# Kernel optimization log

Hardware: AMD Instinct MI355X
Metric: run time of the kernel (lower is better)

Reference implementation:

```python
import jax, jax.numpy as jnp
import numpy as np

N_NODES = 50000
N_EDGES = 400000
F_IN = 128
HID = 64
HEADS = 8
N_CLASSES = 16
NEG_SLOPE = 0.2  # PyG GATConv default negative_slope


def _glorot(key, shape):
    fan_in, fan_out = shape[0], shape[-1]
    lim = jnp.sqrt(6.0 / (fan_in + fan_out))
    return jax.random.uniform(key, shape, jnp.float32, -lim, lim)


def setup_inputs() -> dict:
    key = jax.random.key(0)
    ks = jax.random.split(key, 16)
    x = jax.random.normal(ks[0], (N_NODES, F_IN), jnp.float32)
    edge_index = jax.random.randint(ks[1], (2, N_EDGES), 0, N_NODES, jnp.int64)
    # layer 0: F_IN -> HEADS*HID (concat)
    W0 = _glorot(ks[2], (F_IN, HEADS * HID))
    a_s0 = _glorot(ks[3], (HEADS, HID))
    a_d0 = _glorot(ks[4], (HEADS, HID))
    b0 = jnp.zeros((HEADS * HID,), jnp.float32)
    # layer 1: HEADS*HID -> HEADS*HID (concat)
    W1 = _glorot(ks[5], (HEADS * HID, HEADS * HID))
    a_s1 = _glorot(ks[6], (HEADS, HID))
    a_d1 = _glorot(ks[7], (HEADS, HID))
    b1 = jnp.zeros((HEADS * HID,), jnp.float32)
    # final layer: HEADS*HID -> N_CLASSES, heads=1, concat=False (mean over heads)
    W2 = _glorot(ks[8], (HEADS * HID, 1 * N_CLASSES))
    a_s2 = _glorot(ks[9], (1, N_CLASSES))
    a_d2 = _glorot(ks[10], (1, N_CLASSES))
    b2 = jnp.zeros((N_CLASSES,), jnp.float32)
    return {"x": x, "edge_index": edge_index,
            "W0": W0, "a_s0": a_s0, "a_d0": a_d0, "b0": b0,
            "W1": W1, "a_s1": a_s1, "a_d1": a_d1, "b1": b1,
            "W2": W2, "a_s2": a_s2, "a_d2": a_d2, "b2": b2}


def gat_conv(x, src, dst, W, a_src, a_dst, b, num_nodes, concat):
    """One PyG-style GATConv (self-loops already in src/dst).
    x: [N, F_in]; W: [F_in, H*C]; a_src/a_dst: [H, C]; b: [H*C] or [C]."""
    H, C = a_src.shape
    h = (x @ W).reshape(num_nodes, H, C)                    # [N,H,C]
    al_s = jnp.einsum('nhc,hc->nh', h, a_src)               # [N,H]
    al_d = jnp.einsum('nhc,hc->nh', h, a_dst)               # [N,H]
    e = jax.nn.leaky_relu(al_s[src] + al_d[dst], NEG_SLOPE) # [E,H]
    # scatter-softmax over incoming edges of each destination node
    m = jax.ops.segment_max(e, dst, num_segments=num_nodes)  # [N,H]
    ex = jnp.exp(e - m[dst])
    denom = jax.ops.segment_sum(ex, dst, num_segments=num_nodes)
    alpha = ex / denom[dst]                                  # [E,H]
    out = jax.ops.segment_sum(alpha[:, :, None] * h[src], dst,
                              num_segments=num_nodes)        # [N,H,C]
    if concat:
        return out.reshape(num_nodes, H * C) + b
    return out.mean(axis=1) + b


def reference(x, edge_index, W0, a_s0, a_d0, b0, W1, a_s1, a_d1, b1,
              W2, a_s2, a_d2, b2):
    N = x.shape[0]
    # PyG GATConv adds self-loops by default
    loops = jnp.arange(N, dtype=edge_index.dtype)
    src = jnp.concatenate([edge_index[0], loops])
    dst = jnp.concatenate([edge_index[1], loops])
    h = gat_conv(x, src, dst, W0, a_s0, a_d0, b0, N, concat=True)
    h = jax.nn.elu(h)  # dropout is identity in eval mode
    h = gat_conv(h, src, dst, W1, a_s1, a_d1, b1, N, concat=True)
    h = jax.nn.elu(h)
    return gat_conv(h, src, dst, W2, a_s2, a_d2, b2, N, concat=False)
```

## Files before the change

kernel.cpp:

```cpp
#include <hip/hip_runtime.h>

#define N_NODES 50000
#define N_EDGES 400000
#define E_TOT   450000
#define NEG 0.2f
#define NB_SCAN ((N_NODES + 255) / 256)
#define MAXD 64

typedef unsigned short ushort_t;
typedef __attribute__((ext_vector_type(8))) _Float16 half8;
typedef __attribute__((ext_vector_type(4))) float  f32x4;
typedef __attribute__((ext_vector_type(8))) unsigned short ushort8;

__device__ __forceinline__ ushort_t f2h(float f){
    _Float16 h = (_Float16)f;
    union { _Float16 h; ushort_t u; } v; v.h = h; return v.u;
}
__device__ __forceinline__ float h_lo(unsigned u){
    union { unsigned u; _Float16 h[2]; } v; v.u = u; return (float)v.h[0];
}
__device__ __forceinline__ float h_hi(unsigned u){
    union { unsigned u; _Float16 h[2]; } v; v.u = u; return (float)v.h[1];
}
__device__ __forceinline__ void gload_lds16(const void* g, void* l){
    __builtin_amdgcn_global_load_lds((const __attribute__((address_space(1))) void*)g,
                                     (__attribute__((address_space(3))) void*)l, 16, 0, 0);
}
__device__ __forceinline__ int wave_incl_scan(int v, int lane){
    #pragma unroll
    for(int off = 1; off < 64; off <<= 1){
        int t = __shfl_up(v, off, 64);
        if(lane >= off) v += t;
    }
    return v;
}


__global__ void cvt_all(const float* __restrict__ x, const float* __restrict__ W0,
                        const float* __restrict__ W1, const float* __restrict__ W2,
                        const int* __restrict__ ei,
                        ushort_t* __restrict__ xbf, ushort_t* __restrict__ W0t,
                        ushort_t* __restrict__ W1t, ushort_t* __restrict__ W2t,
                        int* __restrict__ deg){
    int i = blockIdx.x*256 + threadIdx.x;
    if(i < N_NODES*128) xbf[i] = f2h(x[i]);
    if(i < 512*128){ int n = i >> 7, k = i & 127; W0t[i] = f2h(W0[(size_t)k*512 + n]); }
    if(i < 512*512){ int n = i >> 9, k = i & 511; W1t[i] = f2h(W1[(size_t)k*512 + n]); }
    if(i < 16*512){ int n = i >> 9, k = i & 511; W2t[i] = f2h(W2[(size_t)k*16 + n]); }
    if(i < E_TOT){
        int dst = (i < N_EDGES) ? ei[N_EDGES + i] : (i - N_EDGES);
        atomicAdd(&deg[dst], 1);
    }
}


__global__ void deg_block_sum(const int* __restrict__ deg, int* __restrict__ bsum){
    int i = blockIdx.x*256 + threadIdx.x;
    int lane = threadIdx.x & 63, wave = threadIdx.x >> 6;
    int v = (i < N_NODES) ? deg[i] : 0;
    #pragma unroll
    for(int off = 1; off < 64; off <<= 1) v += __shfl_xor(v, off, 64);
    __shared__ int sw[4];
    if(lane == 0) sw[wave] = v;
    __syncthreads();
    if(threadIdx.x == 0) bsum[blockIdx.x] = sw[0] + sw[1] + sw[2] + sw[3];
}

__global__ void scan_apply(const int* __restrict__ bsum,
                           int* __restrict__ dw, int* __restrict__ rowptr){
    __shared__ int soff;
    __shared__ int sw[4];
    int i = blockIdx.x*256 + threadIdx.x;
    int lane = threadIdx.x & 63, wave = threadIdx.x >> 6;
    if(wave == 0){
        int s = 0;
        for(int j = lane; j < (int)blockIdx.x; j += 64) s += bsum[j];
        #pragma unroll
        for(int off = 1; off < 64; off <<= 1) s += __shfl_xor(s, off, 64);
        if(lane == 0) soff = s;
    }
    int v = (i < N_NODES) ? dw[i] : 0;
    int incl = wave_incl_scan(v, lane);
    if(lane == 63) sw[wave] = incl;
    __syncthreads();
    int add = soff;
    for(int w = 0; w < wave; w++) add += sw[w];
    int excl = incl - v + add;
    if(i < N_NODES){ rowptr[i] = excl; dw[i] = excl; }
    if(i == N_NODES-1) rowptr[N_NODES] = excl + v;
}

__global__ void scatter_edges(const int* __restrict__ ei, int* __restrict__ wofs,
                              int* __restrict__ csr){
    int e = blockIdx.x*256 + threadIdx.x;
    if(e >= E_TOT) return;
    int src, dst;
    if(e < N_EDGES){ src = ei[e]; dst = ei[N_EDGES + e]; }
    else { src = dst = e - N_EDGES; }
    int pos = atomicAdd(&wofs[dst], 1);
    csr[pos] = src;
}


template<int K>
__global__ __launch_bounds__(256) void gemm_bt(const ushort_t* __restrict__ A,
                                               const ushort_t* __restrict__ Bt,
                                               ushort_t* __restrict__ Cb,
                                               const float* __restrict__ a_s,
                                               const float* __restrict__ a_d,
                                               float* __restrict__ als,
                                               float* __restrict__ ald, int M){
    __shared__ ushort_t As[128*32];
    __shared__ ushort_t Bs[128*32];
    int tid  = threadIdx.x;
    int wave = tid >> 6, lane = tid & 63;
    int wm = wave & 1, wn = wave >> 1;
    int row0 = blockIdx.y * 128;
    int col0 = blockIdx.x * 128;

    f32x4 acc[4][4] = {};

    int lrow = lane >> 2;
    int lchk = (lane & 3) * 8;

    for(int kt = 0; kt < K; kt += 32){
        #pragma unroll
        for(int s = 0; s < 2; s++){
            int seg = wave*2 + s;
            int ar = row0 + seg*16 + lrow;
            ar = ar < M ? ar : M-1;
            gload_lds16(A  + (size_t)ar*K + kt + lchk, As + seg*512);
            int br = col0 + seg*16 + lrow;
            gload_lds16(Bt + (size_t)br*K + kt + lchk, Bs + seg*512);
        }
        __syncthreads();

        half8 a[4], b[4];
        int fm = lane & 15, fq = (lane >> 4) * 8;
        #pragma unroll
        for(int t = 0; t < 4; t++){
            a[t] = *(const half8*)&As[(wm*64 + t*16 + fm)*32 + fq];
            b[t] = *(const half8*)&Bs[(wn*64 + t*16 + fm)*32 + fq];
        }
        #pragma unroll
        for(int i = 0; i < 4; i++)
            #pragma unroll
            for(int j = 0; j < 4; j++)
                acc[i][j] = __builtin_amdgcn_mfma_f32_16x16x32_f16(a[i], b[j], acc[i][j], 0, 0, 0);
        __syncthreads();
    }

    int cm = (lane >> 4) * 4, cn = lane & 15;
    int head = (col0 + wn*64) >> 6;
    float as_[4], ad_[4];
    #pragma unroll
    for(int j = 0; j < 4; j++){
        int c = head*64 + cn + j*16;
        as_[j] = a_s[c]; ad_[j] = a_d[c];
    }
    #pragma unroll
    for(int i = 0; i < 4; i++){
        #pragma unroll
        for(int p = 0; p < 4; p++){
            int r = row0 + wm*64 + i*16 + cm + p;
            float ps = 0.f, pd = 0.f;
            if(r < M){
                ushort_t* cp = &Cb[(size_t)r*512 + col0 + wn*64 + cn];
                #pragma unroll
                for(int j = 0; j < 4; j++){
                    float v = acc[i][j][p];
                    cp[j*16] = f2h(v);
                    ps += v*as_[j]; pd += v*ad_[j];
                }
            }
            #pragma unroll
            for(int off = 1; off < 16; off <<= 1){
                ps += __shfl_xor(ps, off);
                pd += __shfl_xor(pd, off);
            }
            if(cn == 0 && r < M){ als[r*8 + head] = ps; ald[r*8 + head] = pd; }
        }
    }
}


template<int K>
__global__ __launch_bounds__(512, 2) void gemm_bt8(const ushort_t* __restrict__ A,
                                                   const ushort_t* __restrict__ Bt,
                                                   ushort_t* __restrict__ Cb,
                                                   const float* __restrict__ a_s,
                                                   const float* __restrict__ a_d,
                                                   float* __restrict__ als,
                                                   float* __restrict__ ald, int M){
    extern __shared__ ushort_t lds[];
    constexpr int NT = K / 64;
    int tid = threadIdx.x, wave = tid >> 6, lane = tid & 63;
    int wm = wave >> 2, wn = wave & 3;

    int s = blockIdx.x, nb = gridDim.x;
    int cc = s & 7, kk = s >> 3;
    int q = nb >> 3, rr = nb & 7;
    int t = (cc < rr ? cc*(q+1) : rr*(q+1) + (cc-rr)*q) + kk;
    int row0 = (t >> 1) * 256;
    int col0 = (t & 1) * 256;

    int lr = lane >> 3;
    int cs8 = ((lane & 7) ^ lr) << 3;
    int arows[4], brows[4];
    #pragma unroll
    for(int i = 0; i < 4; i++){
        int r = row0 + (wave << 5) + (i << 3) + lr;
        arows[i] = r < M ? r : M-1;
        brows[i] = col0 + (wave << 5) + (i << 3) + lr;
    }

    int l15 = lane & 15, fq = lane >> 4;
    int xr = (lane & 7) << 4;
    int xco0 = ((fq << 4)      ) ^ xr;
    int xco1 = (64 | (fq << 4)) ^ xr;

    f32x4 acc[8][4] = {};

    auto stage = [&](int nbuf, int kt, int i){
        ushort_t* la = lds + nbuf*16384 + (wave << 11) + (i << 9);
        ushort_t* lb = lds + 32768 + nbuf*16384 + (wave << 11) + (i << 9);
        gload_lds16(A  + (size_t)arows[i]*K + kt + cs8, la);
        gload_lds16(Bt + (size_t)brows[i]*K + kt + cs8, lb);
    };

    #pragma unroll
    for(int i = 0; i < 4; i++) stage(0, 0, i);

    for(int it = 0; it < NT; ++it){
        int b = it & 1;
        asm volatile("s_waitcnt vmcnt(0)" ::: "memory");
        __builtin_amdgcn_s_barrier();
        const char* Ac = (const char*)(lds + b*16384);
        const char* Bc = (const char*)(lds + 32768 + b*16384);
        #pragma unroll
        for(int p = 0; p < 4; ++p){
            if(it < NT-1 && p < 2){
                stage(b ^ 1, (it + 1) << 6, 2*p);
                stage(b ^ 1, (it + 1) << 6, 2*p + 1);
            }
            half8 aF[2][2], bF[4][2];
            #pragma unroll
            for(int m2 = 0; m2 < 2; m2++){
                int ro = (((wm << 7) + (((p << 1) | m2) << 4) + l15)) << 7;
                aF[m2][0] = *(const half8*)(Ac + ro + xco0);
                aF[m2][1] = *(const half8*)(Ac + ro + xco1);
            }
            #pragma unroll
            for(int nj = 0; nj < 4; nj++){
                int ro = (((wn << 6) + (nj << 4) + l15)) << 7;
                bF[nj][0] = *(const half8*)(Bc + ro + xco0);
                bF[nj][1] = *(const half8*)(Bc + ro + xco1);
            }
            __builtin_amdgcn_s_barrier();
            __builtin_amdgcn_s_setprio(1);
            #pragma unroll
            for(int m2 = 0; m2 < 2; m2++)
                #pragma unroll
                for(int nj = 0; nj < 4; nj++){
                    acc[(p<<1)|m2][nj] = __builtin_amdgcn_mfma_f32_16x16x32_f16(aF[m2][0], bF[nj][0], acc[(p<<1)|m2][nj], 0, 0, 0);
                    acc[(p<<1)|m2][nj] = __builtin_amdgcn_mfma_f32_16x16x32_f16(aF[m2][1], bF[nj][1], acc[(p<<1)|m2][nj], 0, 0, 0);
                }
            __builtin_amdgcn_s_setprio(0);
            __builtin_amdgcn_s_barrier();
        }
    }

    int head = (col0 >> 6) + wn;
    float asv[4], adv[4];
    #pragma unroll
    for(int nj = 0; nj < 4; nj++){
        int c = (head << 6) + (nj << 4) + l15;
        asv[nj] = a_s[c]; adv[nj] = a_d[c];
    }
    #pragma unroll
    for(int mi = 0; mi < 8; mi++){
        #pragma unroll
        for(int p2 = 0; p2 < 4; p2++){
            int r = row0 + (wm << 7) + (mi << 4) + (fq << 2) + p2;
            float ps = 0.f, pd = 0.f;
            if(r < M){
                ushort_t* cp = &Cb[(size_t)r*512 + (head << 6) + l15];
                #pragma unroll
                for(int nj = 0; nj < 4; nj++){
                    float v = acc[mi][nj][p2];
                    cp[nj << 4] = f2h(v);
                    ps += v*asv[nj]; pd += v*adv[nj];
                }
            }
            #pragma unroll
            for(int off = 1; off < 16; off <<= 1){
                ps += __shfl_xor(ps, off);
                pd += __shfl_xor(pd, off);
            }
            if(l15 == 0 && r < M){ als[r*8 + head] = ps; ald[r*8 + head] = pd; }
        }
    }
}


__global__ __launch_bounds__(256) void attn_agg(const ushort_t* __restrict__ h,
        const float* __restrict__ als, const float* __restrict__ ald,
        const int* __restrict__ rowptr, const int* __restrict__ csr,
        const float* __restrict__ bias, ushort_t* __restrict__ out){
    __shared__ float sm[4][8], sd[4][8];
    __shared__ float sex[4][MAXD][8];
    int wv = threadIdx.x >> 6, lane = threadIdx.x & 63;
    int n = blockIdx.x*4 + wv;
    int start = rowptr[n], end = rowptr[n+1];

    int hd = lane & 7, e8 = lane >> 3;
    float aldv = ald[n*8 + hd];
    float lmax = -1e30f;
    for(int idx = start + e8; idx < end; idx += 8){
        int e = idx - start;
        int src = csr[idx];
        float v = als[src*8 + hd] + aldv;
        v = v > 0.f ? v : NEG*v;
        if(e < MAXD) sex[wv][e][hd] = v;
        lmax = fmaxf(lmax, v);
    }
    for(int off = 8; off < 64; off <<= 1) lmax = fmaxf(lmax, __shfl_xor(lmax, off));
    float lsum = 0.f;
    for(int idx = start + e8; idx < end; idx += 8){
        int e = idx - start;
        float v;
        if(e < MAXD) v = sex[wv][e][hd];
        else { int src = csr[idx]; v = als[src*8 + hd] + aldv; v = v > 0.f ? v : NEG*v; }
        float ex = __expf(v - lmax);
        if(e < MAXD) sex[wv][e][hd] = ex;
        lsum += ex;
    }
    for(int off = 8; off < 64; off <<= 1) lsum += __shfl_xor(lsum, off);
    if(lane < 8){ sm[wv][hd] = lmax; sd[wv][hd] = 1.f / lsum; }
    __syncthreads();

    int head = lane >> 3;
    float inv = sd[wv][head];
    float acc[8] = {};

    int cnt = end - start;
    int nmain = cnt < MAXD ? cnt : MAXD;
    int mend = start + nmain;
    int last = mend - 1;
    for(int idx = start; idx < mend; idx += 8){
        int ss[8]; uint4 pp[8]; float ee[8];
        #pragma unroll
        for(int k = 0; k < 8; k++){
            int j = idx + k;
            ss[k] = csr[j <= last ? j : last];
        }
        #pragma unroll
        for(int k = 0; k < 8; k++)
            pp[k] = *(const uint4*)&h[(size_t)ss[k]*512 + lane*8];
        #pragma unroll
        for(int k = 0; k < 8; k++){
            int j = idx + k;
            ee[k] = (j < mend) ? sex[wv][j-start][head] : 0.f;
        }
        #pragma unroll
        for(int k = 0; k < 8; k++){
            acc[0] += ee[k]*h_lo(pp[k].x); acc[1] += ee[k]*h_hi(pp[k].x);
            acc[2] += ee[k]*h_lo(pp[k].y); acc[3] += ee[k]*h_hi(pp[k].y);
            acc[4] += ee[k]*h_lo(pp[k].z); acc[5] += ee[k]*h_hi(pp[k].z);
            acc[6] += ee[k]*h_lo(pp[k].w); acc[7] += ee[k]*h_hi(pp[k].w);
        }
    }
    if(mend < end){
        float m = sm[wv][head];
        float aldn = ald[n*8 + head];
        for(int idx = mend; idx < end; idx++){
            int src = csr[idx];
            float v = als[src*8 + head] + aldn;
            v = v > 0.f ? v : NEG*v;
            float e0 = __expf(v - m);
            uint4 p = *(const uint4*)&h[(size_t)src*512 + lane*8];
            acc[0] += e0*h_lo(p.x); acc[1] += e0*h_hi(p.x);
            acc[2] += e0*h_lo(p.y); acc[3] += e0*h_hi(p.y);
            acc[4] += e0*h_lo(p.z); acc[5] += e0*h_hi(p.z);
            acc[6] += e0*h_lo(p.w); acc[7] += e0*h_hi(p.w);
        }
    }

    ushort8 o;
    #pragma unroll
    for(int j = 0; j < 8; j++){
        float v = acc[j]*inv + bias[lane*8 + j];
        v = v > 0.f ? v : (__expf(v) - 1.f);
        o[j] = f2h(v);
    }
    *(ushort8*)&out[(size_t)n*512 + lane*8] = o;
}


__global__ __launch_bounds__(256) void gemm2_mfma(const ushort_t* __restrict__ A,
                                                  const ushort_t* __restrict__ W2t,
                                                  const float* __restrict__ a_s2,
                                                  const float* __restrict__ a_d2,
                                                  float* __restrict__ C,
                                                  float* __restrict__ als,
                                                  float* __restrict__ ald){
    int wave = threadIdx.x >> 6, lane = threadIdx.x & 63;
    long row0 = (long)(blockIdx.x*4 + wave)*16;
    int fr = lane & 15, fq = lane >> 4;
    long ar = row0 + fr;
    if(ar > N_NODES-1) ar = N_NODES-1;
    const ushort_t* ap = A + ar*512 + fq*8;
    const ushort_t* bp = W2t + (size_t)fr*512 + fq*8;
    f32x4 acc = {};
    #pragma unroll
    for(int kt = 0; kt < 512; kt += 32){
        half8 a = *(const half8*)(ap + kt);
        half8 b = *(const half8*)(bp + kt);
        acc = __builtin_amdgcn_mfma_f32_16x16x32_f16(a, b, acc, 0, 0, 0);
    }
    float as_ = a_s2[fr], ad_ = a_d2[fr];
    #pragma unroll
    for(int p = 0; p < 4; p++){
        long r = row0 + fq*4 + p;
        float v = acc[p];
        float ps = v*as_, pd = v*ad_;
        #pragma unroll
        for(int off = 1; off < 16; off <<= 1){
            ps += __shfl_xor(ps, off);
            pd += __shfl_xor(pd, off);
        }
        if(r < N_NODES){
            C[r*16 + fr] = v;
            if(fr == 0){ als[r] = ps; ald[r] = pd; }
        }
    }
}

__global__ __launch_bounds__(256) void attn_agg2(const float* __restrict__ h2,
        const float* __restrict__ als, const float* __restrict__ ald,
        const int* __restrict__ rowptr, const int* __restrict__ csr,
        const float* __restrict__ b2, float* __restrict__ out){
    __shared__ float sex2[16][MAXD+1];
    int wv = threadIdx.x >> 6, lane = threadIdx.x & 63;
    int q = lane >> 4, c = lane & 15;
    int slot = wv*4 + q;
    int n = blockIdx.x*16 + slot;
    int start = rowptr[n], end = rowptr[n+1];
    float aldv = ald[n];
    int cnt = end - start;
    int nmain = cnt < MAXD ? cnt : MAXD;
    int mend = start + nmain;

    float lmax = -1e30f;
    for(int idx = start + c; idx < end; idx += 16){
        int e = idx - start;
        float v = als[csr[idx]] + aldv; v = v > 0.f ? v : NEG*v;
        if(e < MAXD) sex2[slot][e] = v;
        lmax = fmaxf(lmax, v);
    }
    #pragma unroll
    for(int off = 1; off < 16; off <<= 1) lmax = fmaxf(lmax, __shfl_xor(lmax, off));
    float lsum = 0.f;
    for(int idx = start + c; idx < end; idx += 16){
        int e = idx - start;
        float v;
        if(e < MAXD) v = sex2[slot][e];
        else { v = als[csr[idx]] + aldv; v = v > 0.f ? v : NEG*v; }
        float ex = __expf(v - lmax);
        if(e < MAXD) sex2[slot][e] = ex;
        lsum += ex;
    }
    #pragma unroll
    for(int off = 1; off < 16; off <<= 1) lsum += __shfl_xor(lsum, off);
    float inv = 1.f / lsum;

    float acc = 0.f;
    for(int idx = start; idx < mend; idx++){
        int src = csr[idx];
        float ex = sex2[slot][idx - start];
        acc += ex * h2[(size_t)src*16 + c];
    }
    for(int idx = mend; idx < end; idx++){
        int src = csr[idx];
        float v = als[src] + aldv; v = v > 0.f ? v : NEG*v;
        acc += __expf(v - lmax) * h2[(size_t)src*16 + c];
    }
    out[(size_t)n*16 + c] = acc*inv + b2[c];
}


extern "C" void kernel_launch(void* const* d_in, const int* in_sizes, int n_in,
                              void* d_out, int out_size, void* d_ws, size_t ws_size,
                              hipStream_t stream) {
    const float* x    = (const float*)d_in[0];
    const int*   ei   = (const int*)  d_in[1];
    const float* W0   = (const float*)d_in[2];
    const float* a_s0 = (const float*)d_in[3];
    const float* a_d0 = (const float*)d_in[4];
    const float* b0   = (const float*)d_in[5];
    const float* W1   = (const float*)d_in[6];
    const float* a_s1 = (const float*)d_in[7];
    const float* a_d1 = (const float*)d_in[8];
    const float* b1   = (const float*)d_in[9];
    const float* W2   = (const float*)d_in[10];
    const float* a_s2 = (const float*)d_in[11];
    const float* a_d2 = (const float*)d_in[12];
    const float* b2   = (const float*)d_in[13];
    float* out = (float*)d_out;

    char* w = (char*)d_ws;
    auto alloc = [&](size_t bytes){ void* p = (void*)w; w += (bytes + 255) & ~(size_t)255; return p; };
    int*      rowptr = (int*)     alloc((N_NODES+1)*sizeof(int));
    int*      wofs   = (int*)     alloc((N_NODES+1)*sizeof(int));
    int*      bsum   = (int*)     alloc(NB_SCAN*sizeof(int));
    int*      csr    = (int*)     alloc(E_TOT*sizeof(int));
    float*    als    = (float*)   alloc((size_t)N_NODES*8*sizeof(float));
    float*    ald    = (float*)   alloc((size_t)N_NODES*8*sizeof(float));
    float*    als2   = (float*)   alloc((size_t)N_NODES*sizeof(float));
    float*    ald2   = (float*)   alloc((size_t)N_NODES*sizeof(float));
    ushort_t* hb     = (ushort_t*)alloc((size_t)N_NODES*512*sizeof(ushort_t));
    ushort_t* hbf    = (ushort_t*)alloc((size_t)N_NODES*512*sizeof(ushort_t));
    ushort_t* xbf    = (ushort_t*)alloc((size_t)N_NODES*128*sizeof(ushort_t));
    ushort_t* W0t    = (ushort_t*)alloc((size_t)512*128*sizeof(ushort_t));
    ushort_t* W1t    = (ushort_t*)alloc((size_t)512*512*sizeof(ushort_t));
    ushort_t* W2t    = (ushort_t*)alloc((size_t)16*512*sizeof(ushort_t));
    float*    h2     = (float*)   alloc((size_t)N_NODES*16*sizeof(float));

    const int NBLK = 2 * ((N_NODES + 255) / 256);

    (void)hipFuncSetAttribute((const void*)gemm_bt8<512>,
                              hipFuncAttributeMaxDynamicSharedMemorySize, 131072);

    hipMemsetAsync(wofs, 0, (N_NODES+1)*sizeof(int), stream);
    cvt_all<<<(N_NODES*128+255)/256, 256, 0, stream>>>(x, W0, W1, W2, ei, xbf, W0t, W1t, W2t, wofs);

    deg_block_sum<<<NB_SCAN, 256, 0, stream>>>(wofs, bsum);
    scan_apply<<<NB_SCAN, 256, 0, stream>>>(bsum, wofs, rowptr);
    scatter_edges<<<(E_TOT+255)/256, 256, 0, stream>>>(ei, wofs, csr);

    gemm_bt<128><<<dim3(4, (N_NODES+127)/128), 256, 0, stream>>>(xbf, W0t, hb, a_s0, a_d0, als, ald, N_NODES);
    attn_agg<<<N_NODES/4, 256, 0, stream>>>(hb, als, ald, rowptr, csr, b0, hbf);

    gemm_bt8<512><<<NBLK, 512, 131072, stream>>>(hbf, W1t, hb, a_s1, a_d1, als, ald, N_NODES);
    attn_agg<<<N_NODES/4, 256, 0, stream>>>(hb, als, ald, rowptr, csr, b1, hbf);

    gemm2_mfma<<<(N_NODES+63)/64, 256, 0, stream>>>(hbf, W2t, a_s2, a_d2, h2, als2, ald2);
    attn_agg2<<<N_NODES/16, 256, 0, stream>>>(h2, als2, ald2, rowptr, csr, b2, out);
}
```

Measured before the change: 424.3 us.

## Fuse fp32-to-fp16 input conversion into layer-0 GEMM with full-K swizzled LDS tiles

Removes the separate conversion pass that wrote an fp16 copy of x. The layer-0 GEMM now reads fp32 x directly, converts it in registers and stores it to LDS. It also loads the whole K=128 tile at once into XOR-swizzled LDS, which drops the per-k-step barriers. The conversion kernel now launches only enough blocks for edges and weights. Each x tile is re-read in fp32 by the four column blocks, and the larger 64KB LDS footprint may lower occupancy.

Result: no change. 429.3 us (+1.2%).

```diff
diff --git a/kernel.cpp b/kernel.cpp
--- a/kernel.cpp
+++ b/kernel.cpp
@@ -36,14 +36,13 @@
 }
 
 
-__global__ void cvt_all(const float* __restrict__ x, const float* __restrict__ W0,
+__global__ void cvt_all(const float* __restrict__ W0,
                         const float* __restrict__ W1, const float* __restrict__ W2,
                         const int* __restrict__ ei,
-                        ushort_t* __restrict__ xbf, ushort_t* __restrict__ W0t,
+                        ushort_t* __restrict__ W0t,
                         ushort_t* __restrict__ W1t, ushort_t* __restrict__ W2t,
                         int* __restrict__ deg){
     int i = blockIdx.x*256 + threadIdx.x;
-    if(i < N_NODES*128) xbf[i] = f2h(x[i]);
     if(i < 512*128){ int n = i >> 7, k = i & 127; W0t[i] = f2h(W0[(size_t)k*512 + n]); }
     if(i < 512*512){ int n = i >> 9, k = i & 511; W1t[i] = f2h(W1[(size_t)k*512 + n]); }
     if(i < 16*512){ int n = i >> 9, k = i & 511; W2t[i] = f2h(W2[(size_t)k*16 + n]); }
@@ -102,52 +101,72 @@
 }
 
 
-template<int K>
-__global__ __launch_bounds__(256) void gemm_bt(const ushort_t* __restrict__ A,
+__global__ __launch_bounds__(256) void gemm_l0(const float* __restrict__ A,
                                                const ushort_t* __restrict__ Bt,
                                                ushort_t* __restrict__ Cb,
                                                const float* __restrict__ a_s,
                                                const float* __restrict__ a_d,
                                                float* __restrict__ als,
                                                float* __restrict__ ald, int M){
-    __shared__ ushort_t As[128*32];
-    __shared__ ushort_t Bs[128*32];
-    int tid  = threadIdx.x;
-    int wave = tid >> 6, lane = tid & 63;
+    extern __shared__ ushort_t lds[];
+    ushort_t* As = lds;
+    ushort_t* Bs = lds + 128*128;
+    int tid = threadIdx.x, wave = tid >> 6, lane = tid & 63;
     int wm = wave & 1, wn = wave >> 1;
     int row0 = blockIdx.y * 128;
     int col0 = blockIdx.x * 128;
 
+    {
+        int rsub = lane >> 4;
+        int c16  = lane & 15;
+        #pragma unroll
+        for(int i = 0; i < 8; i++){
+            int rl = wave*32 + i*4 + rsub;
+            int br = col0 + rl;
+            int sc = c16 ^ (rl & 7);
+            gload_lds16(Bt + (size_t)br*128 + sc*8, Bs + (wave*32 + i*4)*128);
+        }
+    }
+
+    {
+        int rsub = lane >> 4;
+        int c16  = lane & 15;
+        #pragma unroll
+        for(int j = 0; j < 8; j++){
+            int rl = wave*32 + j*4 + rsub;
+            int gr = row0 + rl; gr = gr < M ? gr : M-1;
+            const float* ap = A + (size_t)gr*128 + c16*8;
+            f32x4 lo = *(const f32x4*)ap;
+            f32x4 hi = *(const f32x4*)(ap + 4);
+            union { _Float16 h[8]; half8 v; } u;
+            u.h[0] = (_Float16)lo[0]; u.h[1] = (_Float16)lo[1];
+            u.h[2] = (_Float16)lo[2]; u.h[3] = (_Float16)lo[3];
+            u.h[4] = (_Float16)hi[0]; u.h[5] = (_Float16)hi[1];
+            u.h[6] = (_Float16)hi[2]; u.h[7] = (_Float16)hi[3];
+            int dc = c16 ^ (rl & 7);
+            *(half8*)&As[(size_t)rl*128 + dc*8] = u.v;
+        }
+    }
+
+    __syncthreads();
+
     f32x4 acc[4][4] = {};
-
-    int lrow = lane >> 2;
-    int lchk = (lane & 3) * 8;
-
-    for(int kt = 0; kt < K; kt += 32){
-        #pragma unroll
-        for(int s = 0; s < 2; s++){
-            int seg = wave*2 + s;
-            int ar = row0 + seg*16 + lrow;
-            ar = ar < M ? ar : M-1;
-            gload_lds16(A  + (size_t)ar*K + kt + lchk, As + seg*512);
-            int br = col0 + seg*16 + lrow;
-            gload_lds16(Bt + (size_t)br*K + kt + lchk, Bs + seg*512);
-        }
-        __syncthreads();
-
+    int fm = lane & 15, fq = lane >> 4;
+    #pragma unroll
+    for(int kt = 0; kt < 4; kt++){
         half8 a[4], b[4];
-        int fm = lane & 15, fq = (lane >> 4) * 8;
         #pragma unroll
         for(int t = 0; t < 4; t++){
-            a[t] = *(const half8*)&As[(wm*64 + t*16 + fm)*32 + fq];
-            b[t] = *(const half8*)&Bs[(wn*64 + t*16 + fm)*32 + fq];
+            int ra = wm*64 + t*16 + fm;
+            a[t] = *(const half8*)&As[ra*128 + (((kt*4 + fq) ^ (ra & 7)))*8];
+            int rb = wn*64 + t*16 + fm;
+            b[t] = *(const half8*)&Bs[rb*128 + (((kt*4 + fq) ^ (rb & 7)))*8];
         }
         #pragma unroll
         for(int i = 0; i < 4; i++)
             #pragma unroll
             for(int j = 0; j < 4; j++)
                 acc[i][j] = __builtin_amdgcn_mfma_f32_16x16x32_f16(a[i], b[j], acc[i][j], 0, 0, 0);
-        __syncthreads();
     }
 
     int cm = (lane >> 4) * 4, cn = lane & 15;
@@ -520,7 +539,6 @@
     float*    ald2   = (float*)   alloc((size_t)N_NODES*sizeof(float));
     ushort_t* hb     = (ushort_t*)alloc((size_t)N_NODES*512*sizeof(ushort_t));
     ushort_t* hbf    = (ushort_t*)alloc((size_t)N_NODES*512*sizeof(ushort_t));
-    ushort_t* xbf    = (ushort_t*)alloc((size_t)N_NODES*128*sizeof(ushort_t));
     ushort_t* W0t    = (ushort_t*)alloc((size_t)512*128*sizeof(ushort_t));
     ushort_t* W1t    = (ushort_t*)alloc((size_t)512*512*sizeof(ushort_t));
     ushort_t* W2t    = (ushort_t*)alloc((size_t)16*512*sizeof(ushort_t));
@@ -530,15 +548,17 @@
 
     (void)hipFuncSetAttribute((const void*)gemm_bt8<512>,
                               hipFuncAttributeMaxDynamicSharedMemorySize, 131072);
+    (void)hipFuncSetAttribute((const void*)gemm_l0,
+                              hipFuncAttributeMaxDynamicSharedMemorySize, 65536);
 
     hipMemsetAsync(wofs, 0, (N_NODES+1)*sizeof(int), stream);
-    cvt_all<<<(N_NODES*128+255)/256, 256, 0, stream>>>(x, W0, W1, W2, ei, xbf, W0t, W1t, W2t, wofs);
+    cvt_all<<<(E_TOT+255)/256, 256, 0, stream>>>(W0, W1, W2, ei, W0t, W1t, W2t, wofs);
 
     deg_block_sum<<<NB_SCAN, 256, 0, stream>>>(wofs, bsum);
     scan_apply<<<NB_SCAN, 256, 0, stream>>>(bsum, wofs, rowptr);
     scatter_edges<<<(E_TOT+255)/256, 256, 0, stream>>>(ei, wofs, csr);
 
-    gemm_bt<128><<<dim3(4, (N_NODES+127)/128), 256, 0, stream>>>(xbf, W0t, hb, a_s0, a_d0, als, ald, N_NODES);
+    gemm_l0<<<dim3(4, (N_NODES+127)/128), 256, 65536, stream>>>(x, W0t, hb, a_s0, a_d0, als, ald, N_NODES);
     attn_agg<<<N_NODES/4, 256, 0, stream>>>(hb, als, ald, rowptr, csr, b0, hbf);
 
     gemm_bt8<512><<<NBLK, 512, 131072, stream>>>(hbf, W1t, hb, a_s1, a_d1, als, ald, N_NODES);
```
